# Performance work log

Measured on AMD Instinct MI355X. Metric: run time of the kernel, lower is better.

Reference implementation:

```python
import jax, jax.numpy as jnp
import numpy as np

# dims
B, T = 64, 512
L = 3                 # number of HMLSTM layers
IN = 512              # per-layer input size (all equal)
D = L * IN            # 1536 total input size
E = 1024              # embedding_size
H1, H2 = 1024, 1024   # linear_sizes
O = 512               # output_size


def setup_inputs() -> dict:
    key = jax.random.key(0)
    ks = jax.random.split(key, 12)
    s = 0.02
    return {
        "x": jax.random.normal(ks[0], (B, T, D), dtype=jnp.float32),
        # gate linears: Linear(sum(input_sizes) -> 1, bias=False), one per layer, stacked [L, D]
        "Wg": jax.random.normal(ks[1], (L, D), dtype=jnp.float32) * s,
        # per-layer embedding linears Linear(IN -> E), stacked [L, E, IN] / [L, E]
        "We": jax.random.normal(ks[2], (L, E, IN), dtype=jnp.float32) * s,
        "be": jax.random.normal(ks[3], (L, E), dtype=jnp.float32) * s,
        # tanh MLP stack
        "W1": jax.random.normal(ks[4], (H1, E), dtype=jnp.float32) * s,
        "b1": jax.random.normal(ks[5], (H1,), dtype=jnp.float32) * s,
        "W2": jax.random.normal(ks[6], (H2, H1), dtype=jnp.float32) * s,
        "b2": jax.random.normal(ks[7], (H2,), dtype=jnp.float32) * s,
        # output head
        "Wo": jax.random.normal(ks[8], (O, H2), dtype=jnp.float32) * s,
        "bo": jax.random.normal(ks[9], (O,), dtype=jnp.float32) * s,
    }


def reference(x, Wg, We, be, W1, b1, W2, b2, Wo, bo):
    b, t, d = x.shape
    h = x.reshape(b * t, d)                       # per-timestep features, fully batched over time
    # gates: sigmoid(Linear(full h -> 1)) per layer -> [N, L]
    g = jax.nn.sigmoid(h @ Wg.T)
    # split full input into per-layer chunks (equal sizes -> reshape) and gate them
    hl = h.reshape(b * t, L, IN) * g[:, :, None]  # [N, L, IN]
    # s = sum_l Linear_l(h_l * g_l); biases sum since each embedding adds its own bias
    s = jnp.einsum("nli,lei->ne", hl, We) + be.sum(axis=0)
    he = jax.nn.relu(s)
    # fnn: tanh-activated linear stack
    o = jnp.tanh(he @ W1.T + b1)
    o = jnp.tanh(o @ W2.T + b2)
    out = o @ Wo.T + bo
    return out.reshape(b, t, O)
```

## Files before the change

kernel.cpp:

```cpp
#include <hip/hip_runtime.h>
#include <math.h>


typedef __attribute__((ext_vector_type(8))) short short8;
typedef __attribute__((ext_vector_type(4))) float float4v;

#define DEV __device__ __forceinline__

DEV unsigned short f2bf(float f){
    union{float f; unsigned int i;} c; c.f = f;
    unsigned int r = c.i + 0x7fffu + ((c.i>>16)&1u);
    return (unsigned short)(r>>16);
}
DEV unsigned int pack2(float a, float b){
    return (unsigned int)f2bf(a) | ((unsigned int)f2bf(b)<<16);
}

DEV void gload_lds16(const unsigned short* g, unsigned short* l){
    __builtin_amdgcn_global_load_lds((const __attribute__((address_space(1))) void*)g,
                                     (__attribute__((address_space(3))) void*)l, 16, 0, 0);
}

__global__ __launch_bounds__(256) void prep(
    const float* __restrict__ x,  const float* __restrict__ Wg,
    const float* __restrict__ W1, const float* __restrict__ W2,
    const float* __restrict__ Wo, const float* __restrict__ We,
    unsigned short* __restrict__ u,   unsigned short* __restrict__ W1b,
    unsigned short* __restrict__ W2b, unsigned short* __restrict__ Wob,
    unsigned short* __restrict__ Wep)
{
    int b = blockIdx.x;
    if(b < 8192){
        int row  = b*4 + (threadIdx.x>>6);
        int lane = threadIdx.x & 63;
        const float4* xr = (const float4*)(x + (size_t)row*1536);
        float4 hv[6];
        #pragma unroll
        for(int j=0;j<6;j++) hv[j] = xr[j*64 + lane];

        float p[3];
        #pragma unroll
        for(int l=0;l<3;l++){
            const float4* wr = (const float4*)(Wg + (size_t)l*1536);
            float s = 0.f;
            #pragma unroll
            for(int j=0;j<6;j++){
                float4 wv = wr[j*64 + lane];
                s += hv[j].x*wv.x + hv[j].y*wv.y + hv[j].z*wv.z + hv[j].w*wv.w;
            }
            p[l] = s;
        }
        #pragma unroll
        for(int off=32; off; off>>=1){
            p[0] += __shfl_xor(p[0], off);
            p[1] += __shfl_xor(p[1], off);
            p[2] += __shfl_xor(p[2], off);
        }
        float g[3];
        #pragma unroll
        for(int l=0;l<3;l++) g[l] = 1.f/(1.f + __expf(-p[l]));

        uint2* ur = (uint2*)(u + (size_t)row*1536);
        #pragma unroll
        for(int j=0;j<6;j++){
            float gj = g[(j*64+lane)>>7];
            uint2 o;
            o.x = pack2(hv[j].x*gj, hv[j].y*gj);
            o.y = pack2(hv[j].z*gj, hv[j].w*gj);
            ur[j*64 + lane] = o;
        }
        return;
    }
    b -= 8192;
    if(b < 1280){
        const float* src; unsigned short* dst; int v0;
        if(b < 512)      { src = W1; dst = W1b; v0 = b<<8; }
        else if(b < 1024){ src = W2; dst = W2b; v0 = (b-512)<<8; }
        else             { src = Wo; dst = Wob; v0 = (b-1024)<<8; }
        int v = v0 + threadIdx.x;
        const float4* s = (const float4*)(src) + (size_t)v*2;
        float4 a = s[0], c = s[1];
        uint4 o;
        o.x = pack2(a.x, a.y); o.y = pack2(a.z, a.w);
        o.z = pack2(c.x, c.y); o.w = pack2(c.z, c.w);
        *((uint4*)dst + v) = o;
        return;
    }
    b -= 1280;
    int v  = b*256 + threadIdx.x;
    int i8 = v & 63;
    int e  = (v>>6) & 1023;
    int l  = v>>16;
    const float4* s = (const float4*)(We + (size_t)l*524288 + (size_t)e*512 + i8*8);
    float4 a = s[0], c = s[1];
    uint4 o;
    o.x = pack2(a.x, a.y); o.y = pack2(a.z, a.w);
    o.z = pack2(c.x, c.y); o.w = pack2(c.z, c.w);
    *(uint4*)(Wep + (size_t)e*1536 + (size_t)l*512 + i8*8) = o;
}

template<int ACT, int BIAS_ROWS, bool F32OUT>
__global__ __launch_bounds__(256, 2) void gemm_bt2(
    const unsigned short* __restrict__ A,
    const unsigned short* __restrict__ W,
    const float* __restrict__ bias,
    void* __restrict__ Cv,
    int M, int N, int K)
{
    __shared__ __align__(128) unsigned short As[2*128*32];
    __shared__ __align__(128) unsigned short Bs[2*256*32];

    const int tid = threadIdx.x;
    const int nb  = N >> 8;
    const int mt  = M >> 7;
    const int xcd = blockIdx.x & 7;
    const int j   = blockIdx.x >> 3;
    const int bm  = xcd*(mt>>3) + j/nb;
    const int bn  = j % nb;
    const int m0  = bm << 7, n0 = bn << 8;

    const int lane = tid & 63, wid = tid >> 6;
    const int lr = lane & 15, quad = lane >> 4;
    const int cread = ((quad ^ (lr & 3)) * 8);
    const int rl  = lane >> 2;
    const int cbl = (lane & 3) ^ (rl & 3);
    const size_t aoff = (size_t)rl*K + cbl*8;
    const int nt = K >> 5;

    float4v acc[8][4];
    #pragma unroll
    for(int i=0;i<8;i++)
        #pragma unroll
        for(int jj=0;jj<4;jj++) acc[i][jj] = (float4v){0.f,0.f,0.f,0.f};

#define STAGE_A(d,s,P) gload_lds16(A + ((size_t)(m0 + (wid*2+(d))*16))*K + (size_t)(s)*32 + aoff, \
                                   &As[(P)*4096 + ((wid*2+(d))*16)*32])
#define STAGE_B(d,s,P) gload_lds16(W + ((size_t)(n0 + (wid*4+(d))*16))*K + (size_t)(s)*32 + aoff, \
                                   &Bs[(P)*8192 + ((wid*4+(d))*16)*32])
#define STAGE_ALL(s,P) do{ STAGE_A(0,s,P); STAGE_A(1,s,P); \
    STAGE_B(0,s,P); STAGE_B(1,s,P); STAGE_B(2,s,P); STAGE_B(3,s,P); }while(0)

#define READ_AF(mi) af[mi] = *(const short8*)&Ap[(mi)*512 + lr*32 + cread]
#define MFMA_MI(mi) do{ \
    acc[mi][0] = __builtin_amdgcn_mfma_f32_16x16x32_bf16(af[mi], bfr[0], acc[mi][0], 0,0,0); \
    acc[mi][1] = __builtin_amdgcn_mfma_f32_16x16x32_bf16(af[mi], bfr[1], acc[mi][1], 0,0,0); \
    acc[mi][2] = __builtin_amdgcn_mfma_f32_16x16x32_bf16(af[mi], bfr[2], acc[mi][2], 0,0,0); \
    acc[mi][3] = __builtin_amdgcn_mfma_f32_16x16x32_bf16(af[mi], bfr[3], acc[mi][3], 0,0,0); }while(0)

    STAGE_ALL(0,0);
    asm volatile("s_waitcnt vmcnt(0)" ::: "memory");
    __builtin_amdgcn_s_barrier();

    for(int tt=0; tt<nt; tt+=2){
        #pragma unroll
        for(int uu=0; uu<2; ++uu){
            const int T = tt + uu;
            if(T+1 < nt) STAGE_ALL(T+1, 1-uu);
            __builtin_amdgcn_sched_barrier(0);

            const unsigned short* Ap = &As[uu*4096];
            const unsigned short* Bp = &Bs[uu*8192 + wid*2048];
            short8 af[8], bfr[4];
            bfr[0] = *(const short8*)&Bp[        lr*32 + cread];
            bfr[1] = *(const short8*)&Bp[ 512 +  lr*32 + cread];
            bfr[2] = *(const short8*)&Bp[1024 +  lr*32 + cread];
            bfr[3] = *(const short8*)&Bp[1536 +  lr*32 + cread];
            READ_AF(0); READ_AF(1); READ_AF(2); READ_AF(3);
            __builtin_amdgcn_s_setprio(1);
            MFMA_MI(0); READ_AF(4);
            MFMA_MI(1); READ_AF(5);
            MFMA_MI(2); READ_AF(6);
            MFMA_MI(3); READ_AF(7);
            MFMA_MI(4); MFMA_MI(5); MFMA_MI(6); MFMA_MI(7);
            __builtin_amdgcn_s_setprio(0);

            if(T+1 < nt){
                asm volatile("s_waitcnt vmcnt(0)" ::: "memory");
                __builtin_amdgcn_s_barrier();
            }
        }
    }
#undef STAGE_A
#undef STAGE_B
#undef STAGE_ALL
#undef READ_AF
#undef MFMA_MI

    #pragma unroll
    for(int ni=0; ni<4; ++ni){
        const int n = n0 + wid*64 + ni*16 + lr;
        float bsum = 0.f;
        #pragma unroll
        for(int r=0; r<BIAS_ROWS; ++r) bsum += bias[(size_t)r*N + n];
        #pragma unroll
        for(int Q=0; Q<8; ++Q){
            #pragma unroll
            for(int reg=0; reg<4; ++reg){
                const int m = m0 + Q*16 + quad*4 + reg;
                float v = acc[Q][ni][reg] + bsum;
                if(ACT==1)      v = fmaxf(v, 0.f);
                else if(ACT==2) v = tanhf(v);
                if constexpr (F32OUT) ((float*)Cv)[(size_t)m*N + n] = v;
                else                  ((unsigned short*)Cv)[(size_t)m*N + n] = f2bf(v);
            }
        }
    }
}

extern "C" void kernel_launch(void* const* d_in, const int* in_sizes, int n_in,
                              void* d_out, int out_size, void* d_ws, size_t ws_size,
                              hipStream_t stream)
{
    const float* x  = (const float*)d_in[0];
    const float* Wg = (const float*)d_in[1];
    const float* We = (const float*)d_in[2];
    const float* be = (const float*)d_in[3];
    const float* W1 = (const float*)d_in[4];
    const float* b1 = (const float*)d_in[5];
    const float* W2 = (const float*)d_in[6];
    const float* b2 = (const float*)d_in[7];
    const float* Wo = (const float*)d_in[8];
    const float* bo = (const float*)d_in[9];
    float* out = (float*)d_out;

    const int M = 32768;

    char* w = (char*)d_ws;
    unsigned short* Wep   = (unsigned short*)w; w += (size_t)1024*1536*2;
    unsigned short* W1b   = (unsigned short*)w; w += (size_t)1024*1024*2;
    unsigned short* W2b   = (unsigned short*)w; w += (size_t)1024*1024*2;
    unsigned short* Wob   = (unsigned short*)w; w += (size_t)512*1024*2;
    unsigned short* slotA = (unsigned short*)w; w += (size_t)M*1536*2;
    unsigned short* slotB = (unsigned short*)w; w += (size_t)M*1024*2;
    unsigned short* u  = slotA;
    unsigned short* o1 = slotA;
    unsigned short* he = slotB;
    unsigned short* o2 = slotB;

    hipLaunchKernelGGL(prep, dim3(10240), dim3(256), 0, stream,
                       x, Wg, W1, W2, Wo, We, u, W1b, W2b, Wob, Wep);

    hipLaunchKernelGGL((gemm_bt2<1,3,false>), dim3((M/128)*(1024/256)), dim3(256), 0, stream,
                       u,  Wep, be, he,  M, 1024, 1536);
    hipLaunchKernelGGL((gemm_bt2<2,1,false>), dim3((M/128)*(1024/256)), dim3(256), 0, stream,
                       he, W1b, b1, o1,  M, 1024, 1024);
    hipLaunchKernelGGL((gemm_bt2<2,1,false>), dim3((M/128)*(1024/256)), dim3(256), 0, stream,
                       o1, W2b, b2, o2,  M, 1024, 1024);
    hipLaunchKernelGGL((gemm_bt2<0,1,true>),  dim3((M/128)*(512/256)),  dim3(256), 0, stream,
                       o2, Wob, bo, out, M, 512, 1024);
}
```

Before: 678.8 us.

## Pre-swizzle weights into MFMA fragment layout and load B directly to registers

```diff
diff --git a/kernel.cpp b/kernel.cpp
--- a/kernel.cpp
+++ b/kernel.cpp
@@ -77,8 +77,14 @@
         if(b < 512)      { src = W1; dst = W1b; v0 = b<<8; }
         else if(b < 1024){ src = W2; dst = W2b; v0 = (b-512)<<8; }
         else             { src = Wo; dst = Wob; v0 = (b-1024)<<8; }
-        int v = v0 + threadIdx.x;
-        const float4* s = (const float4*)(src) + (size_t)v*2;
+        int v  = v0 + threadIdx.x;
+        int l  = v & 63;
+        int f  = v >> 6;
+        int ks = f & 31;
+        int nf = f >> 5;
+        int n  = nf*16 + (l&15);
+        int k  = ks*32 + ((l>>4)<<3);
+        const float4* s = (const float4*)(src + (size_t)n*1024 + k);
         float4 a = s[0], c = s[1];
         uint4 o;
         o.x = pack2(a.x, a.y); o.y = pack2(a.z, a.w);
@@ -87,28 +93,35 @@
         return;
     }
     b -= 1280;
-    int v  = b*256 + threadIdx.x;
-    int i8 = v & 63;
-    int e  = (v>>6) & 1023;
-    int l  = v>>16;
-    const float4* s = (const float4*)(We + (size_t)l*524288 + (size_t)e*512 + i8*8);
-    float4 a = s[0], c = s[1];
-    uint4 o;
-    o.x = pack2(a.x, a.y); o.y = pack2(a.z, a.w);
-    o.z = pack2(c.x, c.y); o.w = pack2(c.z, c.w);
-    *(uint4*)(Wep + (size_t)e*1536 + (size_t)l*512 + i8*8) = o;
+    {
+        int v  = b*256 + threadIdx.x;
+        int l  = v & 63;
+        int f  = v >> 6;
+        int ks = f % 48;
+        int nf = f / 48;
+        int e  = nf*16 + (l&15);
+        int dk = ks*32 + ((l>>4)<<3);
+        int layer = dk >> 9;
+        int i  = dk & 511;
+        const float4* s = (const float4*)(We + (size_t)layer*524288 + (size_t)e*512 + i);
+        float4 a = s[0], c = s[1];
+        uint4 o;
+        o.x = pack2(a.x, a.y); o.y = pack2(a.z, a.w);
+        o.z = pack2(c.x, c.y); o.w = pack2(c.z, c.w);
+        *((uint4*)Wep + v) = o;
+        return;
+    }
 }
 
 template<int ACT, int BIAS_ROWS, bool F32OUT>
-__global__ __launch_bounds__(256, 2) void gemm_bt2(
+__global__ __launch_bounds__(256, 2) void gemm_bd(
     const unsigned short* __restrict__ A,
-    const unsigned short* __restrict__ W,
+    const unsigned short* __restrict__ Wp,
     const float* __restrict__ bias,
     void* __restrict__ Cv,
     int M, int N, int K)
 {
-    __shared__ __align__(128) unsigned short As[2*128*32];
-    __shared__ __align__(128) unsigned short Bs[2*256*32];
+    __shared__ __align__(128) unsigned short As[2*128*64];
 
     const int tid = threadIdx.x;
     const int nb  = N >> 8;
@@ -120,12 +133,14 @@
     const int m0  = bm << 7, n0 = bn << 8;
 
     const int lane = tid & 63, wid = tid >> 6;
-    const int lr = lane & 15, quad = lane >> 4;
-    const int cread = ((quad ^ (lr & 3)) * 8);
-    const int rl  = lane >> 2;
-    const int cbl = (lane & 3) ^ (rl & 3);
-    const size_t aoff = (size_t)rl*K + cbl*8;
-    const int nt = K >> 5;
+    const int lr = lane & 15, quad = lane >> 4, sx = lr & 7;
+    const int srow = lane >> 3;
+    const int scb  = (lane & 7) ^ srow;
+    const size_t aoff = (size_t)srow*K + scb*8;
+    const int KS = K >> 5;
+    const int nf0 = (n0 >> 4) + wid*4;
+    const int nt = K >> 6;
+    const short8* Bfp = (const short8*)Wp;
 
     float4v acc[8][4];
     #pragma unroll
@@ -133,56 +148,91 @@
         #pragma unroll
         for(int jj=0;jj<4;jj++) acc[i][jj] = (float4v){0.f,0.f,0.f,0.f};
 
-#define STAGE_A(d,s,P) gload_lds16(A + ((size_t)(m0 + (wid*2+(d))*16))*K + (size_t)(s)*32 + aoff, \
-                                   &As[(P)*4096 + ((wid*2+(d))*16)*32])
-#define STAGE_B(d,s,P) gload_lds16(W + ((size_t)(n0 + (wid*4+(d))*16))*K + (size_t)(s)*32 + aoff, \
-                                   &Bs[(P)*8192 + ((wid*4+(d))*16)*32])
-#define STAGE_ALL(s,P) do{ STAGE_A(0,s,P); STAGE_A(1,s,P); \
-    STAGE_B(0,s,P); STAGE_B(1,s,P); STAGE_B(2,s,P); STAGE_B(3,s,P); }while(0)
-
-#define READ_AF(mi) af[mi] = *(const short8*)&Ap[(mi)*512 + lr*32 + cread]
-#define MFMA_MI(mi) do{ \
-    acc[mi][0] = __builtin_amdgcn_mfma_f32_16x16x32_bf16(af[mi], bfr[0], acc[mi][0], 0,0,0); \
-    acc[mi][1] = __builtin_amdgcn_mfma_f32_16x16x32_bf16(af[mi], bfr[1], acc[mi][1], 0,0,0); \
-    acc[mi][2] = __builtin_amdgcn_mfma_f32_16x16x32_bf16(af[mi], bfr[2], acc[mi][2], 0,0,0); \
-    acc[mi][3] = __builtin_amdgcn_mfma_f32_16x16x32_bf16(af[mi], bfr[3], acc[mi][3], 0,0,0); }while(0)
+#define STAGE_A(d,s,P) gload_lds16(A + ((size_t)(m0 + wid*32 + (d)*8))*K + (size_t)(s)*64 + aoff, \
+                                   &As[(P)*8192 + (wid*32 + (d)*8)*64])
+#define STAGE_ALL(s,P) do{ STAGE_A(0,s,P); STAGE_A(1,s,P); STAGE_A(2,s,P); STAGE_A(3,s,P); }while(0)
+#define BLOAD(dst, Tt) do{ \
+    _Pragma("unroll") \
+    for(int ni=0; ni<4; ++ni) \
+        _Pragma("unroll") \
+        for(int ks=0; ks<2; ++ks) \
+            dst[ni][ks] = Bfp[((size_t)(nf0+ni)*KS + (Tt)*2 + ks)*64 + lane]; }while(0)
+
+#define READ_AF(s,mi) do{ \
+    af[s][0] = *(const short8*)&Ap[(mi)*1024 + lr*64 + ((quad^sx)*8)]; \
+    af[s][1] = *(const short8*)&Ap[(mi)*1024 + lr*64 + (((4+quad)^sx)*8)]; }while(0)
+#define MFMA_MI(mi,s,bq) do{ \
+    _Pragma("unroll") \
+    for(int ks=0; ks<2; ++ks) \
+        _Pragma("unroll") \
+        for(int ni=0; ni<4; ++ni) \
+            acc[mi][ni] = __builtin_amdgcn_mfma_f32_16x16x32_bf16( \
+                af[s][ks], bq[ni][ks], acc[mi][ni], 0, 0, 0); }while(0)
+
+    short8 bqA[4][2], bqB[4][2];
 
     STAGE_ALL(0,0);
-    asm volatile("s_waitcnt vmcnt(0)" ::: "memory");
+    __builtin_amdgcn_sched_barrier(0);
+    BLOAD(bqA, 0);
+    __builtin_amdgcn_sched_barrier(0);
+    asm volatile("s_waitcnt vmcnt(8)" ::: "memory");
     __builtin_amdgcn_s_barrier();
 
     for(int tt=0; tt<nt; tt+=2){
-        #pragma unroll
-        for(int uu=0; uu<2; ++uu){
-            const int T = tt + uu;
-            if(T+1 < nt) STAGE_ALL(T+1, 1-uu);
+        {
+            const int T = tt;
+            STAGE_ALL(T+1, 1);
             __builtin_amdgcn_sched_barrier(0);
-
-            const unsigned short* Ap = &As[uu*4096];
-            const unsigned short* Bp = &Bs[uu*8192 + wid*2048];
-            short8 af[8], bfr[4];
-            bfr[0] = *(const short8*)&Bp[        lr*32 + cread];
-            bfr[1] = *(const short8*)&Bp[ 512 +  lr*32 + cread];
-            bfr[2] = *(const short8*)&Bp[1024 +  lr*32 + cread];
-            bfr[3] = *(const short8*)&Bp[1536 +  lr*32 + cread];
-            READ_AF(0); READ_AF(1); READ_AF(2); READ_AF(3);
+            BLOAD(bqB, T+1);
+            __builtin_amdgcn_sched_barrier(0);
+
+            const unsigned short* Ap = &As[0];
+            short8 af[4][2];
+            READ_AF(0,0); READ_AF(1,1);
             __builtin_amdgcn_s_setprio(1);
-            MFMA_MI(0); READ_AF(4);
-            MFMA_MI(1); READ_AF(5);
-            MFMA_MI(2); READ_AF(6);
-            MFMA_MI(3); READ_AF(7);
-            MFMA_MI(4); MFMA_MI(5); MFMA_MI(6); MFMA_MI(7);
+            MFMA_MI(0,0,bqA); READ_AF(2,2);
+            MFMA_MI(1,1,bqA); READ_AF(3,3);
+            MFMA_MI(2,2,bqA); READ_AF(0,4);
+            MFMA_MI(3,3,bqA); READ_AF(1,5);
+            MFMA_MI(4,0,bqA); READ_AF(2,6);
+            MFMA_MI(5,1,bqA); READ_AF(3,7);
+            MFMA_MI(6,2,bqA); MFMA_MI(7,3,bqA);
             __builtin_amdgcn_s_setprio(0);
 
-            if(T+1 < nt){
-                asm volatile("s_waitcnt vmcnt(0)" ::: "memory");
+            asm volatile("s_waitcnt vmcnt(8)" ::: "memory");
+            __builtin_amdgcn_s_barrier();
+        }
+        {
+            const int T = tt+1;
+            const bool more = (T+1 < nt);
+            if(more){
+                STAGE_ALL(T+1, 0);
+                __builtin_amdgcn_sched_barrier(0);
+                BLOAD(bqA, T+1);
+                __builtin_amdgcn_sched_barrier(0);
+            }
+            const unsigned short* Ap = &As[8192];
+            short8 af[4][2];
+            READ_AF(0,0); READ_AF(1,1);
+            __builtin_amdgcn_s_setprio(1);
+            MFMA_MI(0,0,bqB); READ_AF(2,2);
+            MFMA_MI(1,1,bqB); READ_AF(3,3);
+            MFMA_MI(2,2,bqB); READ_AF(0,4);
+            MFMA_MI(3,3,bqB); READ_AF(1,5);
+            MFMA_MI(4,0,bqB); READ_AF(2,6);
+            MFMA_MI(5,1,bqB); READ_AF(3,7);
+            MFMA_MI(6,2,bqB); MFMA_MI(7,3,bqB);
+            __builtin_amdgcn_s_setprio(0);
+
+            if(more){
+                asm volatile("s_waitcnt vmcnt(8)" ::: "memory");
                 __builtin_amdgcn_s_barrier();
             }
         }
     }
 #undef STAGE_A
-#undef STAGE_B
 #undef STAGE_ALL
+#undef BLOAD
 #undef READ_AF
 #undef MFMA_MI
 
@@ -240,12 +290,12 @@
     hipLaunchKernelGGL(prep, dim3(10240), dim3(256), 0, stream,
                        x, Wg, W1, W2, Wo, We, u, W1b, W2b, Wob, Wep);
 
-    hipLaunchKernelGGL((gemm_bt2<1,3,false>), dim3((M/128)*(1024/256)), dim3(256), 0, stream,
+    hipLaunchKernelGGL((gemm_bd<1,3,false>), dim3((M/128)*(1024/256)), dim3(256), 0, stream,
                        u,  Wep, be, he,  M, 1024, 1536);
-    hipLaunchKernelGGL((gemm_bt2<2,1,false>), dim3((M/128)*(1024/256)), dim3(256), 0, stream,
+    hipLaunchKernelGGL((gemm_bd<2,1,false>), dim3((M/128)*(1024/256)), dim3(256), 0, stream,
                        he, W1b, b1, o1,  M, 1024, 1024);
-    hipLaunchKernelGGL((gemm_bt2<2,1,false>), dim3((M/128)*(1024/256)), dim3(256), 0, stream,
+    hipLaunchKernelGGL((gemm_bd<2,1,false>), dim3((M/128)*(1024/256)), dim3(256), 0, stream,
                        o1, W2b, b2, o2,  M, 1024, 1024);
-    hipLaunchKernelGGL((gemm_bt2<0,1,true>),  dim3((M/128)*(512/256)),  dim3(256), 0, stream,
+    hipLaunchKernelGGL((gemm_bd<0,1,true>),  dim3((M/128)*(512/256)),  dim3(256), 0, stream,
                        o2, Wob, bo, out, M, 512, 1024);
 }
```

Result: faster. 661.5 us (-2.5%).
